# Performance work log

Measured on AMD Instinct MI355X. Metric: run time of the kernel, lower is better.

## Reference

```python
import jax, jax.numpy as jnp
import numpy as np

B, T, D_IN, H = 32, 1024, 512, 768
FORGET_BIAS = 1.0  # TF LSTMCell default


def lstm_scan(x_tbd, W, b, peep):
    """Run a peephole LSTM over x_tbd [T, B, D]; returns hidden states [T, B, H].

    Matches tf LSTMCell(use_peepholes=True): gate packing (i, j, f, o),
    peepholes on i/f from c_prev and on o from new c, forget_bias added to f.
    """
    h_units = b.shape[0] // 4
    w_i, w_f, w_o = peep[0], peep[1], peep[2]

    def step(carry, xt):
        c, h = carry
        z = jnp.concatenate([xt, h], axis=-1) @ W + b  # [B, 4H]
        i, j, f, o = jnp.split(z, 4, axis=-1)
        i = jax.nn.sigmoid(i + w_i * c)
        f = jax.nn.sigmoid(f + FORGET_BIAS + w_f * c)
        c_new = f * c + i * jnp.tanh(j)
        o = jax.nn.sigmoid(o + w_o * c_new)
        h_new = o * jnp.tanh(c_new)
        return (c_new, h_new), h_new

    bsz = x_tbd.shape[1]
    init = (jnp.zeros((bsz, h_units), x_tbd.dtype),
            jnp.zeros((bsz, h_units), x_tbd.dtype))
    _, hs = jax.lax.scan(step, init, x_tbd)
    return hs


def setup_inputs() -> dict:
    key = jax.random.key(0)
    ks = jax.random.split(key, 6)
    scale = 0.1  # ~ tf.random_uniform_initializer(-0.1, 0.1)
    x = jax.random.normal(ks[0], (B, T, D_IN), dtype=jnp.float32)
    W_fw = jax.random.uniform(ks[1], (D_IN + H, 4 * H), jnp.float32, -scale, scale)
    W_bw = jax.random.uniform(ks[2], (D_IN + H, 4 * H), jnp.float32, -scale, scale)
    b_fw = jnp.zeros((4 * H,), jnp.float32)
    b_bw = jnp.zeros((4 * H,), jnp.float32)
    peep_fw = jax.random.uniform(ks[3], (3, H), jnp.float32, -scale, scale)
    peep_bw = jax.random.uniform(ks[4], (3, H), jnp.float32, -scale, scale)
    return {"x": x, "W_fw": W_fw, "b_fw": b_fw, "peep_fw": peep_fw,
            "W_bw": W_bw, "b_bw": b_bw, "peep_bw": peep_bw}


def reference(x, W_fw, b_fw, peep_fw, W_bw, b_bw, peep_bw):
    x_tbd = jnp.transpose(x, (1, 0, 2))  # [T, B, D]
    hs_fw = lstm_scan(x_tbd, W_fw, b_fw, peep_fw)            # [T, B, H]
    hs_bw = lstm_scan(x_tbd[::-1], W_bw, b_bw, peep_bw)[::-1]  # [T, B, H]
    out = jnp.concatenate([hs_fw, hs_bw], axis=-1)           # [T, B, 2H]
    # static_bidirectional_rnn + reshape -> [B, n_steps, 2*n_hidden]
    return jnp.transpose(out, (1, 0, 2))
```

## Files before the change

kernel.cpp:

```cpp
#include <hip/hip_runtime.h>
#include <stdint.h>

#define TS   1024
#define NB   32
#define DIN  512
#define HU   768
#define KT   1280
#define NWG  32
#define UPW  24
#define NCT  3
#define APAD 1288
#define SPIN_MAX 16384

typedef _Float16 f16x8 __attribute__((ext_vector_type(8)));
typedef float f32x16 __attribute__((ext_vector_type(16)));
typedef unsigned int u32;
typedef unsigned long long u64;
typedef u32 u32x4 __attribute__((ext_vector_type(4)));

__device__ __forceinline__ unsigned short f2h_bits(float f) {
  _Float16 h = (_Float16)f;
  return __builtin_bit_cast(unsigned short, h);
}

__global__ void lstm_init_k(u32* hb_fw, u32* hb_bw, u32* ctrl) {
  int i = blockIdx.x * 256 + threadIdx.x;
  const int HB = NB * HU / 2;
  if (i < HB) hb_fw[i] = 0u;
  else if (i < 2 * HB) hb_bw[i - HB] = 0u;
  else if (i < 2 * HB + 512) ctrl[i - 2 * HB] = 0u;
}

__global__ void lstm_xpose_k(const float* __restrict__ x, unsigned short* __restrict__ xh) {
  int idx = blockIdx.x * 256 + threadIdx.x;
  int d4 = idx & 127;
  int t  = (idx >> 7) & 1023;
  int b  = idx >> 17;
  float4 v = *(const float4*)(x + ((size_t)(b * TS + t) * DIN + d4 * 4));
  ushort4 o;
  o.x = f2h_bits(v.x); o.y = f2h_bits(v.y); o.z = f2h_bits(v.z); o.w = f2h_bits(v.w);
  *(ushort4*)(xh + ((size_t)(t * NB + b) * DIN + d4 * 4)) = o;
}

#define BAR_LGKM() do { asm volatile("s_waitcnt lgkmcnt(0)" ::: "memory"); \
  __builtin_amdgcn_sched_barrier(0); __builtin_amdgcn_s_barrier(); \
  __builtin_amdgcn_sched_barrier(0); } while (0)
#define BAR_VM0() do { asm volatile("s_waitcnt vmcnt(0) lgkmcnt(0)" ::: "memory"); \
  __builtin_amdgcn_sched_barrier(0); __builtin_amdgcn_s_barrier(); \
  __builtin_amdgcn_sched_barrier(0); } while (0)

__global__ __launch_bounds__(256, 1) void lstm_persist_k(
    const float* __restrict__ Wfw, const float* __restrict__ bfw, const float* __restrict__ pfw,
    const float* __restrict__ Wbw, const float* __restrict__ bbw, const float* __restrict__ pbw,
    const unsigned short* __restrict__ xh,
    unsigned short* hb_fw, unsigned short* hb_bw,
    u32* ctrl, float* __restrict__ out)
{
  __shared__ __align__(16) unsigned short As[NB * APAD];
  __shared__ __align__(16) float Zs[4][NB][100];

  const int tid = threadIdx.x;
  const int dir = (blockIdx.x >= NWG) ? 1 : 0;
  const int gg  = blockIdx.x & (NWG - 1);

  const float* W    = dir ? Wbw : Wfw;
  const float* bias = dir ? bbw : bfw;
  const float* peep = dir ? pbw : pfw;
  unsigned short* hbuf = dir ? hb_bw : hb_fw;
  u32* cnt = ctrl + 16 + dir * 128;
  const int u0 = gg * UPW;

  const int lane  = tid & 63;
  const int wq    = tid >> 6;
  const int colc  = lane & 31;
  const int khalf = lane >> 5;
  const int arow  = colc;
  const int hrow  = tid >> 3;
  const int eb    = tid >> 3;

  f16x8 wfr[NCT][20];
#pragma unroll
  for (int ct = 0; ct < NCT; ++ct) {
    const int gcol = (colc & 3) * HU + u0 + 8 * ct + (colc >> 2);
#pragma unroll
    for (int ks = 0; ks < 20; ++ks) {
      const int k0 = wq * 320 + ks * 16 + khalf * 8;
#pragma unroll
      for (int j = 0; j < 8; ++j)
        wfr[ct][ks][j] = (_Float16)W[(size_t)(k0 + j) * 3072 + gcol];
    }
  }

  float bi[3], bj[3], bfc[3], bo[3], pi[3], pfc[3], po[3], cst[3];
#pragma unroll
  for (int q = 0; q < 3; ++q) {
    const int U = u0 + (tid & 7) + 8 * q;
    bi[q] = bias[U]; bj[q] = bias[HU + U]; bfc[q] = bias[2 * HU + U]; bo[q] = bias[3 * HU + U];
    pi[q] = peep[U]; pfc[q] = peep[HU + U]; po[q] = peep[2 * HU + U];
    cst[q] = 0.0f;
  }

  {
    const unsigned short* x0 = xh + (size_t)(dir ? (TS - 1) : 0) * (NB * DIN);
    u32x4 t[8];
#pragma unroll
    for (int k = 0; k < 8; ++k) t[k] = *(const u32x4*)(x0 + (tid + 256 * k) * 8);
#pragma unroll
    for (int k = 0; k < 8; ++k) {
      const int idx = tid + 256 * k;
      *(u32x4*)(&As[(idx >> 6) * APAD + (idx & 63) * 8]) = t[k];
    }
  }
  u32x4 xr[8];

  for (int s = 0; s < TS; ++s) {
    const int t_in = dir ? (TS - 1 - s) : s;
    const u64* hp64 = (const u64*)(hbuf + (s & 1) * (NB * HU));
    u32* hnext32 = (u32*)(hbuf + (((s & 1) ^ 1)) * (NB * HU));

#pragma unroll
    for (int half = 0; half < 2; ++half) {
      u64 hv[12];
#pragma unroll
      for (int q = 0; q < 6; ++q) {
        const int c = (tid & 7) + 8 * (q + 6 * half);
        hv[2 * q]     = __hip_atomic_load(hp64 + hrow * 192 + c * 2,
                                          __ATOMIC_RELAXED, __HIP_MEMORY_SCOPE_AGENT);
        hv[2 * q + 1] = __hip_atomic_load(hp64 + hrow * 192 + c * 2 + 1,
                                          __ATOMIC_RELAXED, __HIP_MEMORY_SCOPE_AGENT);
      }
#pragma unroll
      for (int q = 0; q < 6; ++q) {
        const int kc = 64 + (tid & 7) + 8 * (q + 6 * half);
        *(u64*)(&As[hrow * APAD + kc * 8])     = hv[2 * q];
        *(u64*)(&As[hrow * APAD + kc * 8 + 4]) = hv[2 * q + 1];
      }
    }
    BAR_LGKM();

    f32x16 a0, a1, a2;
#pragma unroll
    for (int r = 0; r < 16; ++r) { a0[r] = 0.f; a1[r] = 0.f; a2[r] = 0.f; }
#pragma unroll
    for (int ks = 0; ks < 20; ++ks) {
      const int kc = wq * 40 + ks * 2 + khalf;
      const f16x8 av = *(const f16x8*)(&As[arow * APAD + kc * 8]);
      a0 = __builtin_amdgcn_mfma_f32_32x32x16_f16(av, wfr[0][ks], a0, 0, 0, 0);
      a1 = __builtin_amdgcn_mfma_f32_32x32x16_f16(av, wfr[1][ks], a1, 0, 0, 0);
      a2 = __builtin_amdgcn_mfma_f32_32x32x16_f16(av, wfr[2][ks], a2, 0, 0, 0);
    }

    if (s + 1 < TS) {
      const int t_next = dir ? (TS - 2 - s) : (s + 1);
      const unsigned short* xnb = xh + (size_t)t_next * (NB * DIN);
#pragma unroll
      for (int k = 0; k < 8; ++k) xr[k] = *(const u32x4*)(xnb + (tid + 256 * k) * 8);
    }

#pragma unroll
    for (int r = 0; r < 16; ++r) {
      const int prow = (r & 3) + 8 * (r >> 2) + 4 * khalf;
      Zs[wq][prow][colc]      = a0[r];
      Zs[wq][prow][32 + colc] = a1[r];
      Zs[wq][prow][64 + colc] = a2[r];
    }
    BAR_LGKM();

    float hn[3];
#pragma unroll
    for (int q = 0; q < 3; ++q) {
      const int uu = (tid & 7) + 8 * q;
      float zi = 0.f, zj = 0.f, zf = 0.f, zo = 0.f;
#pragma unroll
      for (int qq = 0; qq < 4; ++qq) {
        const float4 zp = *(const float4*)(&Zs[qq][eb][uu * 4]);
        zi += zp.x; zj += zp.y; zf += zp.z; zo += zp.w;
      }
      const float ig = 1.f / (1.f + __expf(-(zi + bi[q] + pi[q] * cst[q])));
      const float fg = 1.f / (1.f + __expf(-(zf + bfc[q] + 1.f + pfc[q] * cst[q])));
      const float jt = 1.f - 2.f / (__expf(2.f * (zj + bj[q])) + 1.f);
      const float cn = fg * cst[q] + ig * jt;
      const float og = 1.f / (1.f + __expf(-(zo + bo[q] + po[q] * cn)));
      hn[q] = og * (1.f - 2.f / (__expf(2.f * cn) + 1.f));
      cst[q] = cn;
    }

    if (s < TS - 1) {
#pragma unroll
      for (int q = 0; q < 3; ++q) {
        const u32 mine  = (u32)f2h_bits(hn[q]);
        const u32 other = (u32)(unsigned)__shfl_xor((int)mine, 1, 64);
        if (!(tid & 1)) {
          __hip_atomic_store(hnext32 + ((eb * HU + u0 + (tid & 7) + 8 * q) >> 1),
                             mine | (other << 16),
                             __ATOMIC_RELAXED, __HIP_MEMORY_SCOPE_AGENT);
        }
      }
      BAR_VM0();

      if (tid == 0)
        (void)__hip_atomic_fetch_add(&cnt[(gg >> 2) * 16], 1u,
                                     __ATOMIC_RELAXED, __HIP_MEMORY_SCOPE_AGENT);

#pragma unroll
      for (int q = 0; q < 3; ++q)
        out[((size_t)eb * TS + t_in) * 1536 + dir * HU + u0 + (tid & 7) + 8 * q] = hn[q];

#pragma unroll
      for (int k = 0; k < 8; ++k) {
        const int idx = tid + 256 * k;
        *(u32x4*)(&As[(idx >> 6) * APAD + (idx & 63) * 8]) = xr[k];
      }

      if (wq == 0) {
        const u32 need = 4u * (u32)(s + 1);
        int it = 0; bool ok;
        do {
          u32 v = need;
          if (lane < 8)
            v = __hip_atomic_load(&cnt[lane * 16], __ATOMIC_RELAXED, __HIP_MEMORY_SCOPE_AGENT);
          ok = __all((int)(v >= need));
          if (!ok) __builtin_amdgcn_s_sleep(2);
        } while (!ok && ++it < SPIN_MAX);
      }
      __builtin_amdgcn_sched_barrier(0);
      __builtin_amdgcn_s_barrier();
      __builtin_amdgcn_sched_barrier(0);
    } else {
#pragma unroll
      for (int q = 0; q < 3; ++q)
        out[((size_t)eb * TS + t_in) * 1536 + dir * HU + u0 + (tid & 7) + 8 * q] = hn[q];
    }
  }
}

extern "C" void kernel_launch(void* const* d_in, const int* in_sizes, int n_in,
                              void* d_out, int out_size, void* d_ws, size_t ws_size,
                              hipStream_t stream) {
  const float* x   = (const float*)d_in[0];
  const float* Wfw = (const float*)d_in[1];
  const float* bfw = (const float*)d_in[2];
  const float* pfw = (const float*)d_in[3];
  const float* Wbw = (const float*)d_in[4];
  const float* bbw = (const float*)d_in[5];
  const float* pbw = (const float*)d_in[6];
  float* out = (float*)d_out;

  char* ws = (char*)d_ws;
  unsigned short* xh   = (unsigned short*)ws;
  unsigned short* hbfw = (unsigned short*)(ws + 33554432);
  unsigned short* hbbw = (unsigned short*)(ws + 33554432 + 98304);
  u32* ctrl            = (u32*)(ws + 33554432 + 2 * 98304);

  lstm_init_k<<<97, 256, 0, stream>>>((u32*)hbfw, (u32*)hbbw, ctrl);
  lstm_xpose_k<<<16384, 256, 0, stream>>>(x, xh);
  lstm_persist_k<<<dim3(2 * NWG), dim3(256), 0, stream>>>(Wfw, bfw, pfw, Wbw, bbw, pbw,
                                                          xh, hbfw, hbbw, ctrl, out);
}
```

Before: 5.395 ms.

## Replace counter barrier with step-tagged hidden-state words polled directly

The separate atomic counter and its spin-wait are removed. Each thread now writes its three fp16 hidden values together with a 16-bit step tag as one 64-bit atomic store. Consumers poll the hidden buffer until every tag matches the current step, which takes the vmcnt drain, the counter increment and the second barrier off the per-step critical path. Output stores are deferred by one step and made nontemporal so they overlap with the next step's work. In exchange, consumers spin by reloading the full 32-word row, and the layout now needs repacking from 48-bit groups into LDS.

```diff
diff --git a/kernel.cpp b/kernel.cpp
--- a/kernel.cpp
+++ b/kernel.cpp
@@ -5,12 +5,11 @@
 #define NB   32
 #define DIN  512
 #define HU   768
-#define KT   1280
 #define NWG  32
 #define UPW  24
-#define NCT  3
 #define APAD 1288
-#define SPIN_MAX 16384
+#define HB64 8192
+#define SPIN_MAX (1 << 16)
 
 typedef _Float16 f16x8 __attribute__((ext_vector_type(8)));
 typedef float f32x16 __attribute__((ext_vector_type(16)));
@@ -18,17 +17,13 @@
 typedef unsigned long long u64;
 typedef u32 u32x4 __attribute__((ext_vector_type(4)));
 
-__device__ __forceinline__ unsigned short f2h_bits(float f) {
+__device__ __forceinline__ u32 f2h_bits(float f) {
   _Float16 h = (_Float16)f;
-  return __builtin_bit_cast(unsigned short, h);
-}
-
-__global__ void lstm_init_k(u32* hb_fw, u32* hb_bw, u32* ctrl) {
-  int i = blockIdx.x * 256 + threadIdx.x;
-  const int HB = NB * HU / 2;
-  if (i < HB) hb_fw[i] = 0u;
-  else if (i < 2 * HB) hb_bw[i - HB] = 0u;
-  else if (i < 2 * HB + 512) ctrl[i - 2 * HB] = 0u;
+  return (u32)__builtin_bit_cast(unsigned short, h);
+}
+
+__global__ void lstm_init_k(u32* hb) {
+  hb[blockIdx.x * 256 + threadIdx.x] = 0u;
 }
 
 __global__ void lstm_xpose_k(const float* __restrict__ x, unsigned short* __restrict__ xh) {
@@ -38,14 +33,12 @@
   int b  = idx >> 17;
   float4 v = *(const float4*)(x + ((size_t)(b * TS + t) * DIN + d4 * 4));
   ushort4 o;
-  o.x = f2h_bits(v.x); o.y = f2h_bits(v.y); o.z = f2h_bits(v.z); o.w = f2h_bits(v.w);
+  o.x = (unsigned short)f2h_bits(v.x); o.y = (unsigned short)f2h_bits(v.y);
+  o.z = (unsigned short)f2h_bits(v.z); o.w = (unsigned short)f2h_bits(v.w);
   *(ushort4*)(xh + ((size_t)(t * NB + b) * DIN + d4 * 4)) = o;
 }
 
 #define BAR_LGKM() do { asm volatile("s_waitcnt lgkmcnt(0)" ::: "memory"); \
-  __builtin_amdgcn_sched_barrier(0); __builtin_amdgcn_s_barrier(); \
-  __builtin_amdgcn_sched_barrier(0); } while (0)
-#define BAR_VM0() do { asm volatile("s_waitcnt vmcnt(0) lgkmcnt(0)" ::: "memory"); \
   __builtin_amdgcn_sched_barrier(0); __builtin_amdgcn_s_barrier(); \
   __builtin_amdgcn_sched_barrier(0); } while (0)
 
@@ -53,8 +46,7 @@
     const float* __restrict__ Wfw, const float* __restrict__ bfw, const float* __restrict__ pfw,
     const float* __restrict__ Wbw, const float* __restrict__ bbw, const float* __restrict__ pbw,
     const unsigned short* __restrict__ xh,
-    unsigned short* hb_fw, unsigned short* hb_bw,
-    u32* ctrl, float* __restrict__ out)
+    u64* hb, float* __restrict__ out)
 {
   __shared__ __align__(16) unsigned short As[NB * APAD];
   __shared__ __align__(16) float Zs[4][NB][100];
@@ -66,8 +58,7 @@
   const float* W    = dir ? Wbw : Wfw;
   const float* bias = dir ? bbw : bfw;
   const float* peep = dir ? pbw : pfw;
-  unsigned short* hbuf = dir ? hb_bw : hb_fw;
-  u32* cnt = ctrl + 16 + dir * 128;
+  u64* hbuf = hb + dir * 2 * HB64;
   const int u0 = gg * UPW;
 
   const int lane  = tid & 63;
@@ -77,10 +68,11 @@
   const int arow  = colc;
   const int hrow  = tid >> 3;
   const int eb    = tid >> 3;
-
-  f16x8 wfr[NCT][20];
-#pragma unroll
-  for (int ct = 0; ct < NCT; ++ct) {
+  const int ep    = tid & 7;
+
+  f16x8 wfr[3][20];
+#pragma unroll
+  for (int ct = 0; ct < 3; ++ct) {
     const int gcol = (colc & 3) * HU + u0 + 8 * ct + (colc >> 2);
 #pragma unroll
     for (int ks = 0; ks < 20; ++ks) {
@@ -94,7 +86,7 @@
   float bi[3], bj[3], bfc[3], bo[3], pi[3], pfc[3], po[3], cst[3];
 #pragma unroll
   for (int q = 0; q < 3; ++q) {
-    const int U = u0 + (tid & 7) + 8 * q;
+    const int U = u0 + 3 * ep + q;
     bi[q] = bias[U]; bj[q] = bias[HU + U]; bfc[q] = bias[2 * HU + U]; bo[q] = bias[3 * HU + U];
     pi[q] = peep[U]; pfc[q] = peep[HU + U]; po[q] = peep[2 * HU + U];
     cst[q] = 0.0f;
@@ -111,32 +103,56 @@
       *(u32x4*)(&As[(idx >> 6) * APAD + (idx & 63) * 8]) = t[k];
     }
   }
+
   u32x4 xr[8];
+  float hnPrev[3] = {0.f, 0.f, 0.f};
+  int   tPrev = 0;
 
   for (int s = 0; s < TS; ++s) {
     const int t_in = dir ? (TS - 1 - s) : s;
-    const u64* hp64 = (const u64*)(hbuf + (s & 1) * (NB * HU));
-    u32* hnext32 = (u32*)(hbuf + (((s & 1) ^ 1)) * (NB * HU));
-
-#pragma unroll
-    for (int half = 0; half < 2; ++half) {
-      u64 hv[12];
-#pragma unroll
-      for (int q = 0; q < 6; ++q) {
-        const int c = (tid & 7) + 8 * (q + 6 * half);
-        hv[2 * q]     = __hip_atomic_load(hp64 + hrow * 192 + c * 2,
-                                          __ATOMIC_RELAXED, __HIP_MEMORY_SCOPE_AGENT);
-        hv[2 * q + 1] = __hip_atomic_load(hp64 + hrow * 192 + c * 2 + 1,
-                                          __ATOMIC_RELAXED, __HIP_MEMORY_SCOPE_AGENT);
+    const u64* hsrc = hbuf + (s & 1) * HB64;
+    u64*       hdst = hbuf + (((s + 1) & 1)) * HB64;
+
+    u64 v[32];
+    {
+      const u64* bp = hsrc + hrow * 256 + ep * 32;
+      int it = 0; bool ok;
+      do {
+#pragma unroll
+        for (int k = 0; k < 32; ++k)
+          v[k] = __hip_atomic_load(bp + k, __ATOMIC_RELAXED, __HIP_MEMORY_SCOPE_AGENT);
+        u32 bad = 0;
+#pragma unroll
+        for (int k = 0; k < 32; ++k) bad |= (u32)(v[k] >> 48) ^ (u32)s;
+        ok = __all(bad == 0);
+      } while (!ok && ++it < SPIN_MAX);
+    }
+    {
+      char* dst = (char*)&As[hrow * APAD + 512 + ep * 96];
+#pragma unroll
+      for (int gq = 0; gq < 4; ++gq) {
+        u32 w[12];
+#pragma unroll
+        for (int j = 0; j < 4; ++j) {
+          const u64 a = v[8 * gq + 2 * j], b = v[8 * gq + 2 * j + 1];
+          w[3 * j]     = (u32)a;
+          w[3 * j + 1] = ((u32)(a >> 32) & 0xFFFFu) | ((u32)b << 16);
+          w[3 * j + 2] = (u32)(b >> 16);
+        }
+        u32x4* d4 = (u32x4*)(dst + gq * 48);
+        d4[0] = u32x4{w[0], w[1], w[2],  w[3]};
+        d4[1] = u32x4{w[4], w[5], w[6],  w[7]};
+        d4[2] = u32x4{w[8], w[9], w[10], w[11]};
       }
-#pragma unroll
-      for (int q = 0; q < 6; ++q) {
-        const int kc = 64 + (tid & 7) + 8 * (q + 6 * half);
-        *(u64*)(&As[hrow * APAD + kc * 8])     = hv[2 * q];
-        *(u64*)(&As[hrow * APAD + kc * 8 + 4]) = hv[2 * q + 1];
-      }
     }
     BAR_LGKM();
+
+    if (s > 0) {
+#pragma unroll
+      for (int q = 0; q < 3; ++q)
+        __builtin_nontemporal_store(hnPrev[q],
+            out + ((size_t)eb * TS + tPrev) * 1536 + dir * HU + u0 + 3 * ep + q);
+    }
 
     f32x16 a0, a1, a2;
 #pragma unroll
@@ -169,7 +185,7 @@
     float hn[3];
 #pragma unroll
     for (int q = 0; q < 3; ++q) {
-      const int uu = (tid & 7) + 8 * q;
+      const int uu = 3 * ep + q;
       float zi = 0.f, zj = 0.f, zf = 0.f, zo = 0.f;
 #pragma unroll
       for (int qq = 0; qq < 4; ++qq) {
@@ -186,52 +202,28 @@
     }
 
     if (s < TS - 1) {
-#pragma unroll
-      for (int q = 0; q < 3; ++q) {
-        const u32 mine  = (u32)f2h_bits(hn[q]);
-        const u32 other = (u32)(unsigned)__shfl_xor((int)mine, 1, 64);
-        if (!(tid & 1)) {
-          __hip_atomic_store(hnext32 + ((eb * HU + u0 + (tid & 7) + 8 * q) >> 1),
-                             mine | (other << 16),
-                             __ATOMIC_RELAXED, __HIP_MEMORY_SCOPE_AGENT);
-        }
-      }
-      BAR_VM0();
-
-      if (tid == 0)
-        (void)__hip_atomic_fetch_add(&cnt[(gg >> 2) * 16], 1u,
-                                     __ATOMIC_RELAXED, __HIP_MEMORY_SCOPE_AGENT);
-
-#pragma unroll
-      for (int q = 0; q < 3; ++q)
-        out[((size_t)eb * TS + t_in) * 1536 + dir * HU + u0 + (tid & 7) + 8 * q] = hn[q];
+      const u32 h01 = f2h_bits(hn[0]) | (f2h_bits(hn[1]) << 16);
+      const u32 h2t = f2h_bits(hn[2]) | (((u32)(s + 1)) << 16);
+      __hip_atomic_store(hdst + eb * 256 + 8 * gg + ep,
+                         ((u64)h2t << 32) | (u64)h01,
+                         __ATOMIC_RELAXED, __HIP_MEMORY_SCOPE_AGENT);
 
 #pragma unroll
       for (int k = 0; k < 8; ++k) {
         const int idx = tid + 256 * k;
         *(u32x4*)(&As[(idx >> 6) * APAD + (idx & 63) * 8]) = xr[k];
       }
-
-      if (wq == 0) {
-        const u32 need = 4u * (u32)(s + 1);
-        int it = 0; bool ok;
-        do {
-          u32 v = need;
-          if (lane < 8)
-            v = __hip_atomic_load(&cnt[lane * 16], __ATOMIC_RELAXED, __HIP_MEMORY_SCOPE_AGENT);
-          ok = __all((int)(v >= need));
-          if (!ok) __builtin_amdgcn_s_sleep(2);
-        } while (!ok && ++it < SPIN_MAX);
-      }
-      __builtin_amdgcn_sched_barrier(0);
-      __builtin_amdgcn_s_barrier();
-      __builtin_amdgcn_sched_barrier(0);
-    } else {
-#pragma unroll
-      for (int q = 0; q < 3; ++q)
-        out[((size_t)eb * TS + t_in) * 1536 + dir * HU + u0 + (tid & 7) + 8 * q] = hn[q];
-    }
-  }
+    }
+
+#pragma unroll
+    for (int q = 0; q < 3; ++q) hnPrev[q] = hn[q];
+    tPrev = t_in;
+  }
+
+#pragma unroll
+  for (int q = 0; q < 3; ++q)
+    __builtin_nontemporal_store(hnPrev[q],
+        out + ((size_t)eb * TS + tPrev) * 1536 + dir * HU + u0 + 3 * ep + q);
 }
 
 extern "C" void kernel_launch(void* const* d_in, const int* in_sizes, int n_in,
@@ -247,13 +239,11 @@
   float* out = (float*)d_out;
 
   char* ws = (char*)d_ws;
-  unsigned short* xh   = (unsigned short*)ws;
-  unsigned short* hbfw = (unsigned short*)(ws + 33554432);
-  unsigned short* hbbw = (unsigned short*)(ws + 33554432 + 98304);
-  u32* ctrl            = (u32*)(ws + 33554432 + 2 * 98304);
-
-  lstm_init_k<<<97, 256, 0, stream>>>((u32*)hbfw, (u32*)hbbw, ctrl);
+  unsigned short* xh = (unsigned short*)ws;
+  u64* hb            = (u64*)(ws + 33554432);
+
+  lstm_init_k<<<256, 256, 0, stream>>>((u32*)hb);
   lstm_xpose_k<<<16384, 256, 0, stream>>>(x, xh);
   lstm_persist_k<<<dim3(2 * NWG), dim3(256), 0, stream>>>(Wfw, bfw, pfw, Wbw, bbw, pbw,
-                                                          xh, hbfw, hbbw, ctrl, out);
-}
+                                                          xh, hb, out);
+}
```

Result: slower. 9.761 ms (+80.9%).

## Load recurrent h fragments straight into MFMA registers, skipping LDS staging

Applied to the files above, without the earlier changes.

The K dimension is re-partitioned across waves so each lane's A-fragment for the recurrent part comes directly from global h buffer loads into registers, instead of staging h through LDS behind a barrier. The x part still goes through a smaller LDS buffer, and the MFMAs on x are issued while the h loads are in flight. This removes one LDS round trip and one block barrier from the per-step critical path. Output stores become nontemporal, and the init grid grows slightly to cover the whole ctrl region. Each lane now issues 24 scattered 8-byte atomic loads per step, which raises register pressure and may cost more in memory latency.

```diff
diff --git a/kernel.cpp b/kernel.cpp
--- a/kernel.cpp
+++ b/kernel.cpp
@@ -5,11 +5,9 @@
 #define NB   32
 #define DIN  512
 #define HU   768
-#define KT   1280
 #define NWG  32
 #define UPW  24
-#define NCT  3
-#define APAD 1288
+#define XPAD 520
 #define SPIN_MAX 16384
 
 typedef _Float16 f16x8 __attribute__((ext_vector_type(8)));
@@ -17,10 +15,11 @@
 typedef unsigned int u32;
 typedef unsigned long long u64;
 typedef u32 u32x4 __attribute__((ext_vector_type(4)));
-
-__device__ __forceinline__ unsigned short f2h_bits(float f) {
+typedef u64 u64x2 __attribute__((ext_vector_type(2)));
+
+__device__ __forceinline__ u32 f2h_bits(float f) {
   _Float16 h = (_Float16)f;
-  return __builtin_bit_cast(unsigned short, h);
+  return (u32)__builtin_bit_cast(unsigned short, h);
 }
 
 __global__ void lstm_init_k(u32* hb_fw, u32* hb_bw, u32* ctrl) {
@@ -38,7 +37,8 @@
   int b  = idx >> 17;
   float4 v = *(const float4*)(x + ((size_t)(b * TS + t) * DIN + d4 * 4));
   ushort4 o;
-  o.x = f2h_bits(v.x); o.y = f2h_bits(v.y); o.z = f2h_bits(v.z); o.w = f2h_bits(v.w);
+  o.x = (unsigned short)f2h_bits(v.x); o.y = (unsigned short)f2h_bits(v.y);
+  o.z = (unsigned short)f2h_bits(v.z); o.w = (unsigned short)f2h_bits(v.w);
   *(ushort4*)(xh + ((size_t)(t * NB + b) * DIN + d4 * 4)) = o;
 }
 
@@ -56,7 +56,7 @@
     unsigned short* hb_fw, unsigned short* hb_bw,
     u32* ctrl, float* __restrict__ out)
 {
-  __shared__ __align__(16) unsigned short As[NB * APAD];
+  __shared__ __align__(16) unsigned short As[NB * XPAD];
   __shared__ __align__(16) float Zs[4][NB][100];
 
   const int tid = threadIdx.x;
@@ -75,26 +75,26 @@
   const int colc  = lane & 31;
   const int khalf = lane >> 5;
   const int arow  = colc;
-  const int hrow  = tid >> 3;
   const int eb    = tid >> 3;
-
-  f16x8 wfr[NCT][20];
-#pragma unroll
-  for (int ct = 0; ct < NCT; ++ct) {
+  const int ep    = tid & 7;
+
+  f16x8 wfr[3][20];
+#pragma unroll
+  for (int ct = 0; ct < 3; ++ct) {
     const int gcol = (colc & 3) * HU + u0 + 8 * ct + (colc >> 2);
 #pragma unroll
-    for (int ks = 0; ks < 20; ++ks) {
-      const int k0 = wq * 320 + ks * 16 + khalf * 8;
+    for (int m = 0; m < 20; ++m) {
+      const int k0 = (8 * m + 4 * khalf + wq) * 8;
 #pragma unroll
       for (int j = 0; j < 8; ++j)
-        wfr[ct][ks][j] = (_Float16)W[(size_t)(k0 + j) * 3072 + gcol];
+        wfr[ct][m][j] = (_Float16)W[(size_t)(k0 + j) * 3072 + gcol];
     }
   }
 
   float bi[3], bj[3], bfc[3], bo[3], pi[3], pfc[3], po[3], cst[3];
 #pragma unroll
   for (int q = 0; q < 3; ++q) {
-    const int U = u0 + (tid & 7) + 8 * q;
+    const int U = u0 + ep + 8 * q;
     bi[q] = bias[U]; bj[q] = bias[HU + U]; bfc[q] = bias[2 * HU + U]; bo[q] = bias[3 * HU + U];
     pi[q] = peep[U]; pfc[q] = peep[HU + U]; po[q] = peep[2 * HU + U];
     cst[q] = 0.0f;
@@ -108,46 +108,49 @@
 #pragma unroll
     for (int k = 0; k < 8; ++k) {
       const int idx = tid + 256 * k;
-      *(u32x4*)(&As[(idx >> 6) * APAD + (idx & 63) * 8]) = t[k];
-    }
-  }
+      *(u32x4*)(&As[(idx >> 6) * XPAD + (idx & 63) * 8]) = t[k];
+    }
+  }
+  BAR_LGKM();
+
   u32x4 xr[8];
 
   for (int s = 0; s < TS; ++s) {
     const int t_in = dir ? (TS - 1 - s) : s;
-    const u64* hp64 = (const u64*)(hbuf + (s & 1) * (NB * HU));
+    const u64* hsrc64 = (const u64*)(hbuf + (s & 1) * (NB * HU));
     u32* hnext32 = (u32*)(hbuf + (((s & 1) ^ 1)) * (NB * HU));
 
-#pragma unroll
-    for (int half = 0; half < 2; ++half) {
-      u64 hv[12];
-#pragma unroll
-      for (int q = 0; q < 6; ++q) {
-        const int c = (tid & 7) + 8 * (q + 6 * half);
-        hv[2 * q]     = __hip_atomic_load(hp64 + hrow * 192 + c * 2,
-                                          __ATOMIC_RELAXED, __HIP_MEMORY_SCOPE_AGENT);
-        hv[2 * q + 1] = __hip_atomic_load(hp64 + hrow * 192 + c * 2 + 1,
-                                          __ATOMIC_RELAXED, __HIP_MEMORY_SCOPE_AGENT);
-      }
-#pragma unroll
-      for (int q = 0; q < 6; ++q) {
-        const int kc = 64 + (tid & 7) + 8 * (q + 6 * half);
-        *(u64*)(&As[hrow * APAD + kc * 8])     = hv[2 * q];
-        *(u64*)(&As[hrow * APAD + kc * 8 + 4]) = hv[2 * q + 1];
-      }
-    }
-    BAR_LGKM();
+    u64 hv[24];
+#pragma unroll
+    for (int m = 8; m < 20; ++m) {
+      const int c = 8 * m + 4 * khalf + wq;
+      const int i64 = arow * 192 + (c - 64) * 2;
+      hv[2 * (m - 8)]     = __hip_atomic_load(hsrc64 + i64,
+                                              __ATOMIC_RELAXED, __HIP_MEMORY_SCOPE_AGENT);
+      hv[2 * (m - 8) + 1] = __hip_atomic_load(hsrc64 + i64 + 1,
+                                              __ATOMIC_RELAXED, __HIP_MEMORY_SCOPE_AGENT);
+    }
+    __builtin_amdgcn_sched_barrier(0);
 
     f32x16 a0, a1, a2;
 #pragma unroll
     for (int r = 0; r < 16; ++r) { a0[r] = 0.f; a1[r] = 0.f; a2[r] = 0.f; }
 #pragma unroll
-    for (int ks = 0; ks < 20; ++ks) {
-      const int kc = wq * 40 + ks * 2 + khalf;
-      const f16x8 av = *(const f16x8*)(&As[arow * APAD + kc * 8]);
-      a0 = __builtin_amdgcn_mfma_f32_32x32x16_f16(av, wfr[0][ks], a0, 0, 0, 0);
-      a1 = __builtin_amdgcn_mfma_f32_32x32x16_f16(av, wfr[1][ks], a1, 0, 0, 0);
-      a2 = __builtin_amdgcn_mfma_f32_32x32x16_f16(av, wfr[2][ks], a2, 0, 0, 0);
+    for (int m = 0; m < 8; ++m) {
+      const int c = 8 * m + 4 * khalf + wq;
+      const f16x8 av = *(const f16x8*)(&As[arow * XPAD + c * 8]);
+      a0 = __builtin_amdgcn_mfma_f32_32x32x16_f16(av, wfr[0][m], a0, 0, 0, 0);
+      a1 = __builtin_amdgcn_mfma_f32_32x32x16_f16(av, wfr[1][m], a1, 0, 0, 0);
+      a2 = __builtin_amdgcn_mfma_f32_32x32x16_f16(av, wfr[2][m], a2, 0, 0, 0);
+    }
+
+#pragma unroll
+    for (int m = 8; m < 20; ++m) {
+      u64x2 t; t[0] = hv[2 * (m - 8)]; t[1] = hv[2 * (m - 8) + 1];
+      const f16x8 av = __builtin_bit_cast(f16x8, t);
+      a0 = __builtin_amdgcn_mfma_f32_32x32x16_f16(av, wfr[0][m], a0, 0, 0, 0);
+      a1 = __builtin_amdgcn_mfma_f32_32x32x16_f16(av, wfr[1][m], a1, 0, 0, 0);
+      a2 = __builtin_amdgcn_mfma_f32_32x32x16_f16(av, wfr[2][m], a2, 0, 0, 0);
     }
 
     if (s + 1 < TS) {
@@ -169,7 +172,7 @@
     float hn[3];
 #pragma unroll
     for (int q = 0; q < 3; ++q) {
-      const int uu = (tid & 7) + 8 * q;
+      const int uu = ep + 8 * q;
       float zi = 0.f, zj = 0.f, zf = 0.f, zo = 0.f;
 #pragma unroll
       for (int qq = 0; qq < 4; ++qq) {
@@ -188,10 +191,10 @@
     if (s < TS - 1) {
 #pragma unroll
       for (int q = 0; q < 3; ++q) {
-        const u32 mine  = (u32)f2h_bits(hn[q]);
+        const u32 mine  = f2h_bits(hn[q]);
         const u32 other = (u32)(unsigned)__shfl_xor((int)mine, 1, 64);
         if (!(tid & 1)) {
-          __hip_atomic_store(hnext32 + ((eb * HU + u0 + (tid & 7) + 8 * q) >> 1),
+          __hip_atomic_store(hnext32 + ((eb * HU + u0 + ep + 8 * q) >> 1),
                              mine | (other << 16),
                              __ATOMIC_RELAXED, __HIP_MEMORY_SCOPE_AGENT);
         }
@@ -204,12 +207,13 @@
 
 #pragma unroll
       for (int q = 0; q < 3; ++q)
-        out[((size_t)eb * TS + t_in) * 1536 + dir * HU + u0 + (tid & 7) + 8 * q] = hn[q];
+        __builtin_nontemporal_store(hn[q],
+            out + ((size_t)eb * TS + t_in) * 1536 + dir * HU + u0 + ep + 8 * q);
 
 #pragma unroll
       for (int k = 0; k < 8; ++k) {
         const int idx = tid + 256 * k;
-        *(u32x4*)(&As[(idx >> 6) * APAD + (idx & 63) * 8]) = xr[k];
+        *(u32x4*)(&As[(idx >> 6) * XPAD + (idx & 63) * 8]) = xr[k];
       }
 
       if (wq == 0) {
@@ -223,13 +227,12 @@
           if (!ok) __builtin_amdgcn_s_sleep(2);
         } while (!ok && ++it < SPIN_MAX);
       }
-      __builtin_amdgcn_sched_barrier(0);
-      __builtin_amdgcn_s_barrier();
-      __builtin_amdgcn_sched_barrier(0);
+      BAR_LGKM();
     } else {
 #pragma unroll
       for (int q = 0; q < 3; ++q)
-        out[((size_t)eb * TS + t_in) * 1536 + dir * HU + u0 + (tid & 7) + 8 * q] = hn[q];
+        __builtin_nontemporal_store(hn[q],
+            out + ((size_t)eb * TS + t_in) * 1536 + dir * HU + u0 + ep + 8 * q);
     }
   }
 }
@@ -252,7 +255,7 @@
   unsigned short* hbbw = (unsigned short*)(ws + 33554432 + 98304);
   u32* ctrl            = (u32*)(ws + 33554432 + 2 * 98304);
 
-  lstm_init_k<<<97, 256, 0, stream>>>((u32*)hbfw, (u32*)hbbw, ctrl);
+  lstm_init_k<<<99, 256, 0, stream>>>((u32*)hbfw, (u32*)hbbw, ctrl);
   lstm_xpose_k<<<16384, 256, 0, stream>>>(x, xh);
   lstm_persist_k<<<dim3(2 * NWG), dim3(256), 0, stream>>>(Wfw, bfw, pfw, Wbw, bbw, pbw,
                                                           xh, hbfw, hbbw, ctrl, out);
```

New measurement: 7.091 ms. +31.4%, slower.
